# Optimization experiments

Measured on AMD Instinct MI355X. Metric: run time of the kernel, lower is better.

Reference implementation:

```python
import jax, jax.numpy as jnp
import numpy as np

N_GRAPHS = 4096
HIDDEN = 256
OUT_DIM = 256
STEPS = 6
N_NODES = 524288


def setup_inputs() -> dict:
    key = jax.random.key(0)
    ks = jax.random.split(key, 10)
    node_embeddings = jax.random.normal(ks[0], (N_NODES, HIDDEN), dtype=jnp.float32)
    batch_indices = jnp.sort(jax.random.randint(ks[1], (N_NODES,), 0, N_GRAPHS)).astype(jnp.int64)
    s_ih = 1.0 / np.sqrt(2 * HIDDEN)
    s_hh = 1.0 / np.sqrt(HIDDEN)
    W_ih = jax.random.uniform(ks[2], (4 * HIDDEN, 2 * HIDDEN), jnp.float32, -s_ih, s_ih)
    W_hh = jax.random.uniform(ks[3], (4 * HIDDEN, HIDDEN), jnp.float32, -s_hh, s_hh)
    b_ih = jax.random.uniform(ks[4], (4 * HIDDEN,), jnp.float32, -s_hh, s_hh)
    b_hh = jax.random.uniform(ks[5], (4 * HIDDEN,), jnp.float32, -s_hh, s_hh)
    W1 = jax.random.uniform(ks[6], (HIDDEN, 2 * HIDDEN), jnp.float32, -s_ih, s_ih)
    b1 = jax.random.uniform(ks[7], (HIDDEN,), jnp.float32, -s_ih, s_ih)
    W2 = jax.random.uniform(ks[8], (OUT_DIM, HIDDEN), jnp.float32, -s_hh, s_hh)
    b2 = jax.random.uniform(ks[9], (OUT_DIM,), jnp.float32, -s_hh, s_hh)
    return {"node_embeddings": node_embeddings, "batch_indices": batch_indices,
            "W_ih": W_ih, "W_hh": W_hh, "b_ih": b_ih, "b_hh": b_hh,
            "W1": W1, "b1": b1, "W2": W2, "b2": b2}


def _scatter_softmax(e, idx):
    # per-group numerically stable softmax over nodes
    m = jax.ops.segment_max(e, idx, num_segments=N_GRAPHS)
    ex = jnp.exp(e - m[idx])
    s = jax.ops.segment_sum(ex, idx, num_segments=N_GRAPHS)
    return ex / (s[idx] + 1e-16)


def _lstm_cell(x, h, c, W_ih, W_hh, b_ih, b_hh):
    gates = x @ W_ih.T + b_ih + h @ W_hh.T + b_hh  # (G, 4H)
    i, f, g, o = jnp.split(gates, 4, axis=-1)
    c_new = jax.nn.sigmoid(f) * c + jax.nn.sigmoid(i) * jnp.tanh(g)
    h_new = jax.nn.sigmoid(o) * jnp.tanh(c_new)
    return h_new, c_new


def reference(node_embeddings, batch_indices, W_ih, W_hh, b_ih, b_hh, W1, b1, W2, b2):
    idx = batch_indices.astype(jnp.int32)
    h = jnp.zeros((N_GRAPHS, HIDDEN), jnp.float32)
    c = jnp.zeros((N_GRAPHS, HIDDEN), jnp.float32)
    r = jnp.zeros((N_GRAPHS, HIDDEN), jnp.float32)
    for _ in range(STEPS):
        q = h[idx]                                      # (N, H) gather
        e = jnp.sum(node_embeddings * q, axis=-1)       # (N,)
        a = _scatter_softmax(e, idx)                    # (N,)
        r = jax.ops.segment_sum(a[:, None] * node_embeddings, idx, num_segments=N_GRAPHS)
        x = jnp.concatenate([h, r], axis=-1)            # (G, 2H)
        h, c = _lstm_cell(x, h, c, W_ih, W_hh, b_ih, b_hh)
    g_emb = jnp.concatenate([h, r], axis=-1)            # (G, 2H)
    hdn = jax.nn.relu(g_emb @ W1.T + b1)
    return hdn @ W2.T + b2
```

## Files before the change

### kernel.cpp

```cpp
#include <hip/hip_runtime.h>
#include <hip/hip_bf16.h>
#include <math.h>

#define NG 4096

typedef short bfrag __attribute__((ext_vector_type(8)));
typedef float f32x4 __attribute__((ext_vector_type(4)));

__device__ inline ushort f2bf(float v) {
  union { float f; unsigned u; } a; a.f = v;
  unsigned r = a.u + 0x7fffu + ((a.u >> 16) & 1u);
  return (ushort)(r >> 16);
}
__device__ inline float bf2f(ushort h) {
  union { unsigned u; float f; } a; a.u = ((unsigned)h) << 16;
  return a.f;
}

__global__ void detect_kernel(const int* __restrict__ idx32, int* __restrict__ flag) {
  __shared__ int s;
  int t = threadIdx.x;
  if (t == 0) s = 0;
  __syncthreads();
  int dec = 0;
  for (int i = t; i < 4095; i += 256)
    if (idx32[i + 1] < idx32[i]) dec = 1;
  if (dec) atomicOr(&s, 1);
  __syncthreads();
  if (t == 0) *flag = s ? 2 : 1;
}

__global__ void bounds_kernel(const int* __restrict__ idx32, const int* __restrict__ flag,
                              int* __restrict__ starts, int n) {
  int st = *flag;
  int i = blockIdx.x * blockDim.x + threadIdx.x;
  if (i >= n) return;
  int cur = idx32[(size_t)i * st];
  int prev = (i == 0) ? -1 : idx32[(size_t)(i - 1) * st];
  if (cur != prev)
    for (int g = prev + 1; g <= cur; ++g) starts[g] = i;
  if (i == n - 1)
    for (int g = cur + 1; g <= NG; ++g) starts[g] = n;
}

__global__ void wprep_kernel(const float* __restrict__ W_ih, const float* __restrict__ W_hh,
                             const float* __restrict__ b_ih, const float* __restrict__ b_hh,
                             const float* __restrict__ W1, const float* __restrict__ W2,
                             ushort* __restrict__ Wch, ushort* __restrict__ Wcl,
                             ushort* __restrict__ W1h, ushort* __restrict__ W1l,
                             ushort* __restrict__ W2h, ushort* __restrict__ W2l,
                             float* __restrict__ bcat) {
  int i = blockIdx.x * 256 + threadIdx.x;
  if (i < 524288) {
    int n = i >> 9, k = i & 511;
    int u = ((n >> 7) << 5) | (((n >> 6) & 1) << 4) | (n & 15);
    int q = (n >> 4) & 3;
    int ro = q * 256 + u;
    float w = W_ih[(size_t)ro * 512 + k] + (k < 256 ? W_hh[(size_t)ro * 256 + k] : 0.f);
    ushort hi = f2bf(w);
    Wch[i] = hi; Wcl[i] = f2bf(w - bf2f(hi));
    if (k == 0) bcat[n] = b_ih[ro] + b_hh[ro];
  } else if (i < 524288 + 131072) {
    int t = i - 524288;
    float w = W1[t];
    ushort hi = f2bf(w);
    W1h[t] = hi; W1l[t] = f2bf(w - bf2f(hi));
  } else if (i < 524288 + 131072 + 65536) {
    int t = i - 524288 - 131072;
    float w = W2[t];
    ushort hi = f2bf(w);
    W2h[t] = hi; W2l[t] = f2bf(w - bf2f(hi));
  }
}

__global__ __launch_bounds__(256) void attn0_kernel(const float* __restrict__ emb,
                                                    const int* __restrict__ starts,
                                                    float* __restrict__ cst,
                                                    ushort* __restrict__ hbh, ushort* __restrict__ hbl,
                                                    ushort* __restrict__ rbh, ushort* __restrict__ rbl) {
  int g = blockIdx.x, tid = threadIdx.x;
  cst[(size_t)g * 256 + tid] = 0.f;
  hbh[(size_t)g * 256 + tid] = 0;
  hbl[(size_t)g * 256 + tid] = 0;
  int s = starts[g], e = starts[g + 1];
  if (s >= e) {
    rbh[(size_t)g * 256 + tid] = 0;
    rbl[(size_t)g * 256 + tid] = 0;
    return;
  }
  int wave = tid >> 6, lane = tid & 63;
  float4 R0 = make_float4(0.f, 0.f, 0.f, 0.f), R1 = make_float4(0.f, 0.f, 0.f, 0.f);
  for (int n = s + wave * 2; n < e; n += 8) {
    const float* p0 = emb + (size_t)n * 256 + lane * 4;
    float4 v0 = *(const float4*)p0;
    R0.x += v0.x; R0.y += v0.y; R0.z += v0.z; R0.w += v0.w;
    if (n + 1 < e) {
      float4 v1 = *(const float4*)(p0 + 256);
      R1.x += v1.x; R1.y += v1.y; R1.z += v1.z; R1.w += v1.w;
    }
  }
  R0.x += R1.x; R0.y += R1.y; R0.z += R1.z; R0.w += R1.w;
  __shared__ float redR[4][256];
  *(float4*)&redR[wave][lane * 4] = R0;
  __syncthreads();
  float inv = 1.f / (float)(e - s);
  float Rt = 0.f;
#pragma unroll
  for (int w = 0; w < 4; ++w) Rt += redR[w][tid];
  float rv = Rt * inv;
  ushort hi = f2bf(rv);
  rbh[(size_t)g * 256 + tid] = hi;
  rbl[(size_t)g * 256 + tid] = f2bf(rv - bf2f(hi));
}

__global__ __launch_bounds__(256) void attn_kernel(const float* __restrict__ emb,
                                                   const int* __restrict__ starts,
                                                   const ushort* __restrict__ hbh,
                                                   const ushort* __restrict__ hbl,
                                                   ushort* __restrict__ rbh,
                                                   ushort* __restrict__ rbl) {
  int g = blockIdx.x;
  int s = starts[g], e = starts[g + 1];
  int tid = threadIdx.x;
  if (s >= e) {
    rbh[(size_t)g * 256 + tid] = 0;
    rbl[(size_t)g * 256 + tid] = 0;
    return;
  }
  __shared__ float hs[256];
  __shared__ float redM[4], redS[4];
  __shared__ float redR[4][256];
  hs[tid] = bf2f(hbh[(size_t)g * 256 + tid]) + bf2f(hbl[(size_t)g * 256 + tid]);
  __syncthreads();
  int wave = tid >> 6, lane = tid & 63;
  float4 h4 = *(const float4*)&hs[lane * 4];
  float M0 = -INFINITY, S0 = 0.f, M1 = -INFINITY, S1 = 0.f;
  float4 R0 = make_float4(0.f, 0.f, 0.f, 0.f), R1 = make_float4(0.f, 0.f, 0.f, 0.f);
  for (int n = s + wave * 2; n < e; n += 8) {
    const float* p0 = emb + (size_t)n * 256 + lane * 4;
    float4 v0 = *(const float4*)p0;
    bool has1 = (n + 1) < e;
    float4 v1 = make_float4(0.f, 0.f, 0.f, 0.f);
    if (has1) v1 = *(const float4*)(p0 + 256);
    float d0 = v0.x * h4.x + v0.y * h4.y + v0.z * h4.z + v0.w * h4.w;
    float d1 = v1.x * h4.x + v1.y * h4.y + v1.z * h4.z + v1.w * h4.w;
#pragma unroll
    for (int off = 32; off > 0; off >>= 1) {
      d0 += __shfl_xor(d0, off, 64);
      d1 += __shfl_xor(d1, off, 64);
    }
    if (d0 <= M0) {
      float w = __expf(d0 - M0);
      S0 += w;
      R0.x += w * v0.x; R0.y += w * v0.y; R0.z += w * v0.z; R0.w += w * v0.w;
    } else {
      float cc = __expf(M0 - d0);
      S0 = S0 * cc + 1.f;
      R0.x = R0.x * cc + v0.x; R0.y = R0.y * cc + v0.y;
      R0.z = R0.z * cc + v0.z; R0.w = R0.w * cc + v0.w;
      M0 = d0;
    }
    if (has1) {
      if (d1 <= M1) {
        float w = __expf(d1 - M1);
        S1 += w;
        R1.x += w * v1.x; R1.y += w * v1.y; R1.z += w * v1.z; R1.w += w * v1.w;
      } else {
        float cc = __expf(M1 - d1);
        S1 = S1 * cc + 1.f;
        R1.x = R1.x * cc + v1.x; R1.y = R1.y * cc + v1.y;
        R1.z = R1.z * cc + v1.z; R1.w = R1.w * cc + v1.w;
        M1 = d1;
      }
    }
  }
  if (M1 != -INFINITY) {
    float mm = fmaxf(M0, M1);
    float f0 = __expf(M0 - mm), f1 = __expf(M1 - mm);
    S0 = S0 * f0 + S1 * f1;
    R0.x = R0.x * f0 + R1.x * f1; R0.y = R0.y * f0 + R1.y * f1;
    R0.z = R0.z * f0 + R1.z * f1; R0.w = R0.w * f0 + R1.w * f1;
    M0 = mm;
  }
  if (lane == 0) { redM[wave] = M0; redS[wave] = S0; }
  *(float4*)&redR[wave][lane * 4] = R0;
  __syncthreads();
  float m = fmaxf(fmaxf(redM[0], redM[1]), fmaxf(redM[2], redM[3]));
  float St = 0.f, Rt = 0.f;
#pragma unroll
  for (int w = 0; w < 4; ++w) {
    float mw = redM[w];
    float f = (mw == -INFINITY) ? 0.f : __expf(mw - m);
    St += f * redS[w];
    Rt += f * redR[w][tid];
  }
  float rv = Rt / St;
  ushort hi = f2bf(rv);
  rbh[(size_t)g * 256 + tid] = hi;
  rbl[(size_t)g * 256 + tid] = f2bf(rv - bf2f(hi));
}

#define AP 40
__global__ __launch_bounds__(256) void gemm_mfma(
    const ushort* __restrict__ Ah1, const ushort* __restrict__ Al1,
    const ushort* __restrict__ Ah2, const ushort* __restrict__ Al2,
    const ushort* __restrict__ Bhi, const ushort* __restrict__ Blo,
    const float* __restrict__ bias, float* __restrict__ Cf,
    ushort* __restrict__ Chi, ushort* __restrict__ Clo,
    float* __restrict__ cst, ushort* __restrict__ hoh, ushort* __restrict__ hol,
    int N, int K, int mode) {
  __shared__ ushort sAh[128 * AP], sAl[128 * AP], sBh[128 * AP], sBl[128 * AP];
  const int As = 256;
  int tid = threadIdx.x;
  int wave = tid >> 6, lane = tid & 63;
  int fr = lane & 15, fq = lane >> 4;
  int wm = (wave >> 1) * 64, wn = (wave & 1) * 64;
  int r0 = blockIdx.y * 128, c0 = blockIdx.x * 128;
  int lr = tid >> 2, lk = (tid & 3) * 8;
  const ushort* pbh = Bhi + (size_t)(c0 + lr) * K + lk;
  const ushort* pbl = Blo + (size_t)(c0 + lr) * K + lk;
  size_t rstrB = (size_t)64 * K;
  size_t rowA0 = (size_t)(r0 + lr) * As + lk;
  size_t rowA1 = (size_t)(r0 + lr + 64) * As + lk;
  int lo0 = lr * AP + lk, lo1 = (lr + 64) * AP + lk;
  uint4 a0, a1, a2, a3, b0, b1, b2, b3;
#define LOADT(kt) do { \
    const ushort *qh, *ql; int kk; \
    if ((kt) < As) { qh = Ah1; ql = Al1; kk = (kt); } \
    else { qh = Ah2; ql = Al2; kk = (kt) - As; } \
    a0 = *(const uint4*)(qh + rowA0 + kk); \
    a1 = *(const uint4*)(qh + rowA1 + kk); \
    a2 = *(const uint4*)(ql + rowA0 + kk); \
    a3 = *(const uint4*)(ql + rowA1 + kk); \
    b0 = *(const uint4*)(pbh + (kt)); \
    b1 = *(const uint4*)(pbh + rstrB + (kt)); \
    b2 = *(const uint4*)(pbl + (kt)); \
    b3 = *(const uint4*)(pbl + rstrB + (kt)); \
  } while (0)
#define STORET() do { \
    *(uint4*)&sAh[lo0] = a0; *(uint4*)&sAh[lo1] = a1; \
    *(uint4*)&sAl[lo0] = a2; *(uint4*)&sAl[lo1] = a3; \
    *(uint4*)&sBh[lo0] = b0; *(uint4*)&sBh[lo1] = b1; \
    *(uint4*)&sBl[lo0] = b2; *(uint4*)&sBl[lo1] = b3; \
  } while (0)
  LOADT(0);
  STORET();
  f32x4 acc[4][4] = {};
  for (int k0 = 0; k0 < K; k0 += 32) {
    __syncthreads();
    bool nx = (k0 + 32) < K;
    if (nx) LOADT(k0 + 32);
    bfrag ah[4], al[4], bh[4], bl[4];
#pragma unroll
    for (int t = 0; t < 4; ++t) {
      int ra = (wm + t * 16 + fr) * AP + fq * 8;
      int rb = (wn + t * 16 + fr) * AP + fq * 8;
      ah[t] = *(const bfrag*)&sAh[ra];
      al[t] = *(const bfrag*)&sAl[ra];
      bh[t] = *(const bfrag*)&sBh[rb];
      bl[t] = *(const bfrag*)&sBl[rb];
    }
#pragma unroll
    for (int mt = 0; mt < 4; ++mt)
#pragma unroll
      for (int nt = 0; nt < 4; ++nt) {
        acc[mt][nt] = __builtin_amdgcn_mfma_f32_16x16x32_bf16(ah[mt], bh[nt], acc[mt][nt], 0, 0, 0);
        acc[mt][nt] = __builtin_amdgcn_mfma_f32_16x16x32_bf16(ah[mt], bl[nt], acc[mt][nt], 0, 0, 0);
        acc[mt][nt] = __builtin_amdgcn_mfma_f32_16x16x32_bf16(al[mt], bh[nt], acc[mt][nt], 0, 0, 0);
      }
    __syncthreads();
    if (nx) STORET();
  }
#undef LOADT
#undef STORET
  if (mode == 3) {
    float bv0 = bias[c0 + wn + fr];
    float bv1 = bias[c0 + wn + 16 + fr];
    float bv2 = bias[c0 + wn + 32 + fr];
    float bv3 = bias[c0 + wn + 48 + fr];
    int u = (c0 >> 2) + (wn >> 2) + fr;
#pragma unroll
    for (int mt = 0; mt < 4; ++mt)
#pragma unroll
      for (int rg = 0; rg < 4; ++rg) {
        int m = r0 + wm + mt * 16 + fq * 4 + rg;
        float gi = acc[mt][0][rg] + bv0;
        float gf = acc[mt][1][rg] + bv1;
        float gg = acc[mt][2][rg] + bv2;
        float go = acc[mt][3][rg] + bv3;
        float si = 1.f / (1.f + __expf(-gi));
        float sf = 1.f / (1.f + __expf(-gf));
        float so = 1.f / (1.f + __expf(-go));
        float tg = tanhf(gg);
        size_t ci = (size_t)m * 256 + u;
        float cn = sf * cst[ci] + si * tg;
        cst[ci] = cn;
        float hn = so * tanhf(cn);
        ushort hi = f2bf(hn);
        hoh[ci] = hi;
        hol[ci] = f2bf(hn - bf2f(hi));
      }
    return;
  }
#pragma unroll
  for (int mt = 0; mt < 4; ++mt)
#pragma unroll
    for (int nt = 0; nt < 4; ++nt) {
      int n = c0 + wn + nt * 16 + fr;
      float bv = bias[n];
#pragma unroll
      for (int rg = 0; rg < 4; ++rg) {
        int m = r0 + wm + mt * 16 + fq * 4 + rg;
        float v = acc[mt][nt][rg] + bv;
        if (mode == 2) {
          v = fmaxf(v, 0.f);
          ushort hi = f2bf(v);
          Chi[(size_t)m * N + n] = hi;
          Clo[(size_t)m * N + n] = f2bf(v - bf2f(hi));
        } else {
          Cf[(size_t)m * N + n] = v;
        }
      }
    }
}

extern "C" void kernel_launch(void* const* d_in, const int* in_sizes, int n_in,
                              void* d_out, int out_size, void* d_ws, size_t ws_size,
                              hipStream_t stream) {
  const float* emb   = (const float*)d_in[0];
  const int*   idx32 = (const int*)d_in[1];
  const float* W_ih  = (const float*)d_in[2];
  const float* W_hh  = (const float*)d_in[3];
  const float* b_ih  = (const float*)d_in[4];
  const float* b_hh  = (const float*)d_in[5];
  const float* W1    = (const float*)d_in[6];
  const float* b1    = (const float*)d_in[7];
  const float* W2    = (const float*)d_in[8];
  const float* b2    = (const float*)d_in[9];
  float* out = (float*)d_out;
  int N = in_sizes[1];

  char* ws = (char*)d_ws;
  size_t o = 0;
  auto alloc = [&](size_t bytes) { void* p = ws + o; o = (o + bytes + 255) & ~(size_t)255; return p; };
  int*    flag  = (int*)alloc(4);
  int*    starts= (int*)alloc(((size_t)NG + 1) * 4);
  float*  bcat  = (float*)alloc(1024 * 4);
  ushort* Wch   = (ushort*)alloc((size_t)1024 * 512 * 2);
  ushort* Wcl   = (ushort*)alloc((size_t)1024 * 512 * 2);
  ushort* W1h   = (ushort*)alloc((size_t)256 * 512 * 2);
  ushort* W1l   = (ushort*)alloc((size_t)256 * 512 * 2);
  ushort* W2h   = (ushort*)alloc((size_t)256 * 256 * 2);
  ushort* W2l   = (ushort*)alloc((size_t)256 * 256 * 2);
  float*  c     = (float*)alloc((size_t)NG * 256 * 4);
  ushort* hbh0  = (ushort*)alloc((size_t)NG * 256 * 2);
  ushort* hbl0  = (ushort*)alloc((size_t)NG * 256 * 2);
  ushort* hbh1  = (ushort*)alloc((size_t)NG * 256 * 2);
  ushort* hbl1  = (ushort*)alloc((size_t)NG * 256 * 2);
  ushort* rbh   = (ushort*)alloc((size_t)NG * 256 * 2);
  ushort* rbl   = (ushort*)alloc((size_t)NG * 256 * 2);
  ushort* hdnh  = (ushort*)alloc((size_t)NG * 256 * 2);
  ushort* hdnl  = (ushort*)alloc((size_t)NG * 256 * 2);

  detect_kernel<<<1, 256, 0, stream>>>(idx32, flag);
  bounds_kernel<<<(N + 255) / 256, 256, 0, stream>>>(idx32, flag, starts, N);
  wprep_kernel<<<(524288 + 131072 + 65536) / 256, 256, 0, stream>>>(
      W_ih, W_hh, b_ih, b_hh, W1, W2, Wch, Wcl, W1h, W1l, W2h, W2l, bcat);
  attn0_kernel<<<NG, 256, 0, stream>>>(emb, starts, c, hbh0, hbl0, rbh, rbl);

  for (int s = 0; s < 6; ++s) {
    const ushort* hch = (s & 1) ? hbh1 : hbh0;
    const ushort* hcl = (s & 1) ? hbl1 : hbl0;
    ushort* hnh = (s & 1) ? hbh0 : hbh1;
    ushort* hnl = (s & 1) ? hbl0 : hbl1;
    gemm_mfma<<<dim3(1024 / 128, 4096 / 128), 256, 0, stream>>>(
        hch, hcl, rbh, rbl, Wch, Wcl, bcat,
        (float*)nullptr, (ushort*)nullptr, (ushort*)nullptr,
        c, hnh, hnl, 1024, 512, 3);
    if (s < 5)
      attn_kernel<<<NG, 256, 0, stream>>>(emb, starts, hnh, hnl, rbh, rbl);
  }
  gemm_mfma<<<dim3(256 / 128, 4096 / 128), 256, 0, stream>>>(
      hbh0, hbl0, rbh, rbl, W1h, W1l, b1,
      (float*)nullptr, hdnh, hdnl,
      (float*)nullptr, (ushort*)nullptr, (ushort*)nullptr, 256, 512, 2);
  gemm_mfma<<<dim3(256 / 128, 4096 / 128), 256, 0, stream>>>(
      hdnh, hdnl, hdnh, hdnl, W2h, W2l, b2,
      out, (ushort*)nullptr, (ushort*)nullptr,
      (float*)nullptr, (ushort*)nullptr, (ushort*)nullptr, 256, 256, 0);
}
```

Before: 1.492 ms.

## Cache fp16 embeddings for attention steps and shrink GEMM M-tile to 64

The first attention pass now also writes an fp16 copy of the node embeddings. The five later attention kernels read that copy instead of fp32, which halves their dominant memory traffic. The attention kernel is restructured so each half-wave handles one node row with 8 elements per lane, giving 8 partial softmax states per block. The MFMA GEMM tile is reduced from 128x128 to 64x128 rows, doubling the grid for more parallelism. In exchange it adds a 256MB fp16 write and loses precision in the embeddings used for scores and weighted sums.

```diff
diff --git a/kernel.cpp b/kernel.cpp
--- a/kernel.cpp
+++ b/kernel.cpp
@@ -1,5 +1,6 @@
 #include <hip/hip_runtime.h>
 #include <hip/hip_bf16.h>
+#include <hip/hip_fp16.h>
 #include <math.h>
 
 #define NG 4096
@@ -75,6 +76,7 @@
 
 __global__ __launch_bounds__(256) void attn0_kernel(const float* __restrict__ emb,
                                                     const int* __restrict__ starts,
+                                                    ushort* __restrict__ e16,
                                                     float* __restrict__ cst,
                                                     ushort* __restrict__ hbh, ushort* __restrict__ hbl,
                                                     ushort* __restrict__ rbh, ushort* __restrict__ rbl) {
@@ -93,9 +95,17 @@
   for (int n = s + wave * 2; n < e; n += 8) {
     const float* p0 = emb + (size_t)n * 256 + lane * 4;
     float4 v0 = *(const float4*)p0;
+    union { uint2 u; __half h[4]; } pk0;
+    pk0.h[0] = __float2half_rn(v0.x); pk0.h[1] = __float2half_rn(v0.y);
+    pk0.h[2] = __float2half_rn(v0.z); pk0.h[3] = __float2half_rn(v0.w);
+    *(uint2*)(e16 + (size_t)n * 256 + lane * 4) = pk0.u;
     R0.x += v0.x; R0.y += v0.y; R0.z += v0.z; R0.w += v0.w;
     if (n + 1 < e) {
       float4 v1 = *(const float4*)(p0 + 256);
+      union { uint2 u; __half h[4]; } pk1;
+      pk1.h[0] = __float2half_rn(v1.x); pk1.h[1] = __float2half_rn(v1.y);
+      pk1.h[2] = __float2half_rn(v1.z); pk1.h[3] = __float2half_rn(v1.w);
+      *(uint2*)(e16 + (size_t)(n + 1) * 256 + lane * 4) = pk1.u;
       R1.x += v1.x; R1.y += v1.y; R1.z += v1.z; R1.w += v1.w;
     }
   }
@@ -113,7 +123,7 @@
   rbl[(size_t)g * 256 + tid] = f2bf(rv - bf2f(hi));
 }
 
-__global__ __launch_bounds__(256) void attn_kernel(const float* __restrict__ emb,
+__global__ __launch_bounds__(256) void attn_kernel(const ushort* __restrict__ e16,
                                                    const int* __restrict__ starts,
                                                    const ushort* __restrict__ hbh,
                                                    const ushort* __restrict__ hbl,
@@ -128,69 +138,57 @@
     return;
   }
   __shared__ float hs[256];
-  __shared__ float redM[4], redS[4];
-  __shared__ float redR[4][256];
+  __shared__ float redM[8], redS[8];
+  __shared__ float redR[8][256];
   hs[tid] = bf2f(hbh[(size_t)g * 256 + tid]) + bf2f(hbl[(size_t)g * 256 + tid]);
   __syncthreads();
   int wave = tid >> 6, lane = tid & 63;
-  float4 h4 = *(const float4*)&hs[lane * 4];
-  float M0 = -INFINITY, S0 = 0.f, M1 = -INFINITY, S1 = 0.f;
-  float4 R0 = make_float4(0.f, 0.f, 0.f, 0.f), R1 = make_float4(0.f, 0.f, 0.f, 0.f);
+  int half = lane >> 5, l5 = lane & 31;
+  float h8[8];
+#pragma unroll
+  for (int j = 0; j < 8; ++j) h8[j] = hs[l5 * 8 + j];
+  float M = -1e30f, S = 0.f;
+  float R[8] = {0.f, 0.f, 0.f, 0.f, 0.f, 0.f, 0.f, 0.f};
   for (int n = s + wave * 2; n < e; n += 8) {
-    const float* p0 = emb + (size_t)n * 256 + lane * 4;
-    float4 v0 = *(const float4*)p0;
-    bool has1 = (n + 1) < e;
-    float4 v1 = make_float4(0.f, 0.f, 0.f, 0.f);
-    if (has1) v1 = *(const float4*)(p0 + 256);
-    float d0 = v0.x * h4.x + v0.y * h4.y + v0.z * h4.z + v0.w * h4.w;
-    float d1 = v1.x * h4.x + v1.y * h4.y + v1.z * h4.z + v1.w * h4.w;
-#pragma unroll
-    for (int off = 32; off > 0; off >>= 1) {
-      d0 += __shfl_xor(d0, off, 64);
-      d1 += __shfl_xor(d1, off, 64);
-    }
-    if (d0 <= M0) {
-      float w = __expf(d0 - M0);
-      S0 += w;
-      R0.x += w * v0.x; R0.y += w * v0.y; R0.z += w * v0.z; R0.w += w * v0.w;
+    int row = n + half;
+    int rowc = row < e ? row : (e - 1);
+    union { uint4 u; __half h[8]; } uv;
+    uv.u = *(const uint4*)(e16 + (size_t)rowc * 256 + l5 * 8);
+    float vf[8];
+    float d = 0.f;
+#pragma unroll
+    for (int j = 0; j < 8; ++j) {
+      vf[j] = __half2float(uv.h[j]);
+      d = fmaf(vf[j], h8[j], d);
+    }
+#pragma unroll
+    for (int off = 16; off > 0; off >>= 1) d += __shfl_xor(d, off, 64);
+    if (row >= e) d = -INFINITY;
+    if (d <= M) {
+      float w = __expf(d - M);
+      S += w;
+#pragma unroll
+      for (int j = 0; j < 8; ++j) R[j] = fmaf(w, vf[j], R[j]);
     } else {
-      float cc = __expf(M0 - d0);
-      S0 = S0 * cc + 1.f;
-      R0.x = R0.x * cc + v0.x; R0.y = R0.y * cc + v0.y;
-      R0.z = R0.z * cc + v0.z; R0.w = R0.w * cc + v0.w;
-      M0 = d0;
-    }
-    if (has1) {
-      if (d1 <= M1) {
-        float w = __expf(d1 - M1);
-        S1 += w;
-        R1.x += w * v1.x; R1.y += w * v1.y; R1.z += w * v1.z; R1.w += w * v1.w;
-      } else {
-        float cc = __expf(M1 - d1);
-        S1 = S1 * cc + 1.f;
-        R1.x = R1.x * cc + v1.x; R1.y = R1.y * cc + v1.y;
-        R1.z = R1.z * cc + v1.z; R1.w = R1.w * cc + v1.w;
-        M1 = d1;
-      }
-    }
-  }
-  if (M1 != -INFINITY) {
-    float mm = fmaxf(M0, M1);
-    float f0 = __expf(M0 - mm), f1 = __expf(M1 - mm);
-    S0 = S0 * f0 + S1 * f1;
-    R0.x = R0.x * f0 + R1.x * f1; R0.y = R0.y * f0 + R1.y * f1;
-    R0.z = R0.z * f0 + R1.z * f1; R0.w = R0.w * f0 + R1.w * f1;
-    M0 = mm;
-  }
-  if (lane == 0) { redM[wave] = M0; redS[wave] = S0; }
-  *(float4*)&redR[wave][lane * 4] = R0;
-  __syncthreads();
-  float m = fmaxf(fmaxf(redM[0], redM[1]), fmaxf(redM[2], redM[3]));
+      float cc = __expf(M - d);
+      S = S * cc + 1.f;
+#pragma unroll
+      for (int j = 0; j < 8; ++j) R[j] = fmaf(R[j], cc, vf[j]);
+      M = d;
+    }
+  }
+  int ch = wave * 2 + half;
+  if (l5 == 0) { redM[ch] = M; redS[ch] = S; }
+#pragma unroll
+  for (int j = 0; j < 8; ++j) redR[ch][l5 * 8 + j] = R[j];
+  __syncthreads();
+  float m = -1e30f;
+#pragma unroll
+  for (int w = 0; w < 8; ++w) m = fmaxf(m, redM[w]);
   float St = 0.f, Rt = 0.f;
 #pragma unroll
-  for (int w = 0; w < 4; ++w) {
-    float mw = redM[w];
-    float f = (mw == -INFINITY) ? 0.f : __expf(mw - m);
+  for (int w = 0; w < 8; ++w) {
+    float f = __expf(redM[w] - m);
     St += f * redS[w];
     Rt += f * redR[w][tid];
   }
@@ -209,59 +207,58 @@
     ushort* __restrict__ Chi, ushort* __restrict__ Clo,
     float* __restrict__ cst, ushort* __restrict__ hoh, ushort* __restrict__ hol,
     int N, int K, int mode) {
-  __shared__ ushort sAh[128 * AP], sAl[128 * AP], sBh[128 * AP], sBl[128 * AP];
+  __shared__ ushort sAh[64 * AP], sAl[64 * AP], sBh[128 * AP], sBl[128 * AP];
   const int As = 256;
   int tid = threadIdx.x;
   int wave = tid >> 6, lane = tid & 63;
   int fr = lane & 15, fq = lane >> 4;
-  int wm = (wave >> 1) * 64, wn = (wave & 1) * 64;
-  int r0 = blockIdx.y * 128, c0 = blockIdx.x * 128;
+  int wm = (wave >> 1) * 32, wn = (wave & 1) * 64;
+  int r0 = blockIdx.y * 64, c0 = blockIdx.x * 128;
   int lr = tid >> 2, lk = (tid & 3) * 8;
   const ushort* pbh = Bhi + (size_t)(c0 + lr) * K + lk;
   const ushort* pbl = Blo + (size_t)(c0 + lr) * K + lk;
   size_t rstrB = (size_t)64 * K;
-  size_t rowA0 = (size_t)(r0 + lr) * As + lk;
-  size_t rowA1 = (size_t)(r0 + lr + 64) * As + lk;
+  size_t rowA = (size_t)(r0 + lr) * As + lk;
   int lo0 = lr * AP + lk, lo1 = (lr + 64) * AP + lk;
-  uint4 a0, a1, a2, a3, b0, b1, b2, b3;
+  uint4 a0, a2, b0, b1, b2, b3;
 #define LOADT(kt) do { \
     const ushort *qh, *ql; int kk; \
     if ((kt) < As) { qh = Ah1; ql = Al1; kk = (kt); } \
     else { qh = Ah2; ql = Al2; kk = (kt) - As; } \
-    a0 = *(const uint4*)(qh + rowA0 + kk); \
-    a1 = *(const uint4*)(qh + rowA1 + kk); \
-    a2 = *(const uint4*)(ql + rowA0 + kk); \
-    a3 = *(const uint4*)(ql + rowA1 + kk); \
+    a0 = *(const uint4*)(qh + rowA + kk); \
+    a2 = *(const uint4*)(ql + rowA + kk); \
     b0 = *(const uint4*)(pbh + (kt)); \
     b1 = *(const uint4*)(pbh + rstrB + (kt)); \
     b2 = *(const uint4*)(pbl + (kt)); \
     b3 = *(const uint4*)(pbl + rstrB + (kt)); \
   } while (0)
 #define STORET() do { \
-    *(uint4*)&sAh[lo0] = a0; *(uint4*)&sAh[lo1] = a1; \
-    *(uint4*)&sAl[lo0] = a2; *(uint4*)&sAl[lo1] = a3; \
+    *(uint4*)&sAh[lo0] = a0; *(uint4*)&sAl[lo0] = a2; \
     *(uint4*)&sBh[lo0] = b0; *(uint4*)&sBh[lo1] = b1; \
     *(uint4*)&sBl[lo0] = b2; *(uint4*)&sBl[lo1] = b3; \
   } while (0)
   LOADT(0);
   STORET();
-  f32x4 acc[4][4] = {};
+  f32x4 acc[2][4] = {};
   for (int k0 = 0; k0 < K; k0 += 32) {
     __syncthreads();
     bool nx = (k0 + 32) < K;
     if (nx) LOADT(k0 + 32);
-    bfrag ah[4], al[4], bh[4], bl[4];
-#pragma unroll
-    for (int t = 0; t < 4; ++t) {
+    bfrag ah[2], al[2], bh[4], bl[4];
+#pragma unroll
+    for (int t = 0; t < 2; ++t) {
       int ra = (wm + t * 16 + fr) * AP + fq * 8;
-      int rb = (wn + t * 16 + fr) * AP + fq * 8;
       ah[t] = *(const bfrag*)&sAh[ra];
       al[t] = *(const bfrag*)&sAl[ra];
+    }
+#pragma unroll
+    for (int t = 0; t < 4; ++t) {
+      int rb = (wn + t * 16 + fr) * AP + fq * 8;
       bh[t] = *(const bfrag*)&sBh[rb];
       bl[t] = *(const bfrag*)&sBl[rb];
     }
 #pragma unroll
-    for (int mt = 0; mt < 4; ++mt)
+    for (int mt = 0; mt < 2; ++mt)
 #pragma unroll
       for (int nt = 0; nt < 4; ++nt) {
         acc[mt][nt] = __builtin_amdgcn_mfma_f32_16x16x32_bf16(ah[mt], bh[nt], acc[mt][nt], 0, 0, 0);
@@ -280,7 +277,7 @@
     float bv3 = bias[c0 + wn + 48 + fr];
     int u = (c0 >> 2) + (wn >> 2) + fr;
 #pragma unroll
-    for (int mt = 0; mt < 4; ++mt)
+    for (int mt = 0; mt < 2; ++mt)
 #pragma unroll
       for (int rg = 0; rg < 4; ++rg) {
         int m = r0 + wm + mt * 16 + fq * 4 + rg;
@@ -303,7 +300,7 @@
     return;
   }
 #pragma unroll
-  for (int mt = 0; mt < 4; ++mt)
+  for (int mt = 0; mt < 2; ++mt)
 #pragma unroll
     for (int nt = 0; nt < 4; ++nt) {
       int n = c0 + wn + nt * 16 + fr;
@@ -361,30 +358,31 @@
   ushort* rbl   = (ushort*)alloc((size_t)NG * 256 * 2);
   ushort* hdnh  = (ushort*)alloc((size_t)NG * 256 * 2);
   ushort* hdnl  = (ushort*)alloc((size_t)NG * 256 * 2);
+  ushort* e16   = (ushort*)alloc((size_t)N * 256 * 2);
 
   detect_kernel<<<1, 256, 0, stream>>>(idx32, flag);
   bounds_kernel<<<(N + 255) / 256, 256, 0, stream>>>(idx32, flag, starts, N);
   wprep_kernel<<<(524288 + 131072 + 65536) / 256, 256, 0, stream>>>(
       W_ih, W_hh, b_ih, b_hh, W1, W2, Wch, Wcl, W1h, W1l, W2h, W2l, bcat);
-  attn0_kernel<<<NG, 256, 0, stream>>>(emb, starts, c, hbh0, hbl0, rbh, rbl);
+  attn0_kernel<<<NG, 256, 0, stream>>>(emb, starts, e16, c, hbh0, hbl0, rbh, rbl);
 
   for (int s = 0; s < 6; ++s) {
     const ushort* hch = (s & 1) ? hbh1 : hbh0;
     const ushort* hcl = (s & 1) ? hbl1 : hbl0;
     ushort* hnh = (s & 1) ? hbh0 : hbh1;
     ushort* hnl = (s & 1) ? hbl0 : hbl1;
-    gemm_mfma<<<dim3(1024 / 128, 4096 / 128), 256, 0, stream>>>(
+    gemm_mfma<<<dim3(1024 / 128, 4096 / 64), 256, 0, stream>>>(
         hch, hcl, rbh, rbl, Wch, Wcl, bcat,
         (float*)nullptr, (ushort*)nullptr, (ushort*)nullptr,
         c, hnh, hnl, 1024, 512, 3);
     if (s < 5)
-      attn_kernel<<<NG, 256, 0, stream>>>(emb, starts, hnh, hnl, rbh, rbl);
-  }
-  gemm_mfma<<<dim3(256 / 128, 4096 / 128), 256, 0, stream>>>(
+      attn_kernel<<<NG, 256, 0, stream>>>(e16, starts, hnh, hnl, rbh, rbl);
+  }
+  gemm_mfma<<<dim3(256 / 128, 4096 / 64), 256, 0, stream>>>(
       hbh0, hbl0, rbh, rbl, W1h, W1l, b1,
       (float*)nullptr, hdnh, hdnl,
       (float*)nullptr, (ushort*)nullptr, (ushort*)nullptr, 256, 512, 2);
-  gemm_mfma<<<dim3(256 / 128, 4096 / 128), 256, 0, stream>>>(
+  gemm_mfma<<<dim3(256 / 128, 4096 / 64), 256, 0, stream>>>(
       hdnh, hdnl, hdnh, hdnl, W2h, W2l, b2,
       out, (ushort*)nullptr, (ushort*)nullptr,
       (float*)nullptr, (ushort*)nullptr, (ushort*)nullptr, 256, 256, 0);
```

Result: faster. 1.201 ms (-19.5%).
